# Kernel tuning notes

Hardware: AMD Instinct MI355X
Metric: run time of the kernel (lower is better)

The kernel has to match this reference:

```python
import jax, jax.numpy as jnp
import numpy as np

NUM_USERS = 60000
NUM_ITEMS = 40000
NUM_NODES = NUM_USERS + NUM_ITEMS
EMBED_DIM = 64
NUM_LAYERS = 3
NUM_EDGES = 1200000
BATCH = 16384


def setup_inputs() -> dict:
    key = jax.random.key(0)
    ks = jax.random.split(key, 7)
    user_indices = jax.random.randint(ks[0], (BATCH,), 0, NUM_USERS)
    item_indices = jax.random.randint(ks[1], (BATCH,), 0, NUM_ITEMS)
    edge_rows = jax.random.randint(ks[2], (NUM_EDGES,), 0, NUM_NODES)
    edge_cols = jax.random.randint(ks[3], (NUM_EDGES,), 0, NUM_NODES)
    # normalized adjacency values are small positives ~ 1/sqrt(deg_i*deg_j)
    edge_vals = jax.random.uniform(ks[4], (NUM_EDGES,), dtype=jnp.float32) * 0.1
    # xavier_uniform for Embedding(num, dim): bound = sqrt(6/(num+dim))
    bu = float(np.sqrt(6.0 / (NUM_USERS + EMBED_DIM)))
    bi = float(np.sqrt(6.0 / (NUM_ITEMS + EMBED_DIM)))
    user_emb = jax.random.uniform(ks[5], (NUM_USERS, EMBED_DIM), jnp.float32, -bu, bu)
    item_emb = jax.random.uniform(ks[6], (NUM_ITEMS, EMBED_DIM), jnp.float32, -bi, bi)
    return {
        "user_indices": user_indices,
        "item_indices": item_indices,
        "edge_rows": edge_rows,
        "edge_cols": edge_cols,
        "edge_vals": edge_vals,
        "user_emb": user_emb,
        "item_emb": item_emb,
    }


def _spmm(edge_rows, edge_cols, edge_vals, x):
    # out[i] = sum_{e: rows[e]==i} vals[e] * x[cols[e]]  -- COO SpMM
    msgs = edge_vals[:, None] * x[edge_cols]  # [E, D]
    return jax.ops.segment_sum(msgs, edge_rows, num_segments=NUM_NODES)


def reference(user_indices, item_indices, edge_rows, edge_cols, edge_vals,
              user_emb, item_emb):
    all_embeds = jnp.concatenate([user_emb, item_emb], axis=0)  # [N, D]
    for _ in range(NUM_LAYERS):
        all_embeds = _spmm(edge_rows, edge_cols, edge_vals, all_embeds)
    all_users = all_embeds[:NUM_USERS]
    all_items = all_embeds[NUM_USERS:]
    u = all_users[user_indices]  # [B, D]
    v = all_items[item_indices]  # [B, D]
    return jnp.sum(u * v, axis=1)  # [B]
```

## Files before the change

### kernel.cpp

```cpp
#include <hip/hip_runtime.h>

#define NUM_USERS 60000
#define NUM_ITEMS 40000
#define NUM_NODES 100000
#define DIM       64
#define NUM_EDGES 1200000
#define BATCH     16384

#define BROWS 128
#define NBUCK 782
#define CAP   2048
#define EPB   4096
#define NBINS 2048
#define NFLAGW 3125

__device__ __forceinline__ unsigned short f2bf(float f) {
    unsigned u = __float_as_uint(f);
    unsigned r = (u + 0x7FFFu + ((u >> 16) & 1u)) >> 16;
    return (unsigned short)r;
}

__global__ __launch_bounds__(256) void convert_emb(
    const float4* __restrict__ ue, const float4* __restrict__ ie,
    ushort4* __restrict__ xc)
{
    const int nU4 = NUM_USERS * (DIM / 4);
    const int total4 = NUM_NODES * (DIM / 4);
    int i = blockIdx.x * blockDim.x + threadIdx.x;
    int stride = gridDim.x * blockDim.x;
    for (; i < total4; i += stride) {
        float4 v = (i < nU4) ? ue[i] : ie[i - nU4];
        ushort4 s;
        s.x = f2bf(v.x); s.y = f2bf(v.y); s.z = f2bf(v.z); s.w = f2bf(v.w);
        xc[i] = s;
    }
}

__global__ __launch_bounds__(256) void bin_edges(
    const int* __restrict__ rows, const int* __restrict__ cols,
    const float* __restrict__ vals,
    const int* __restrict__ uidx, const int* __restrict__ iidx,
    int* __restrict__ gcursor, unsigned* __restrict__ flags,
    unsigned long long* __restrict__ tmp)
{
    __shared__ int cnt[NBUCK], lcur[NBUCK], gbase[NBUCK];
    int t = threadIdx.x;
    for (int i = t; i < NBUCK; i += 256) { cnt[i] = 0; lcur[i] = 0; }
    int fbase = blockIdx.x * 112;
    for (int k = t; k < 112; k += 256) {
        int gi = fbase + k;
        if (gi < BATCH) {
            int n = uidx[gi];
            atomicOr(&flags[n >> 5], 1u << (n & 31));
        } else if (gi < 2 * BATCH) {
            int n = NUM_USERS + iidx[gi - BATCH];
            atomicOr(&flags[n >> 5], 1u << (n & 31));
        }
    }
    __syncthreads();
    int base = blockIdx.x * EPB;
    int lim = NUM_EDGES - base; if (lim > EPB) lim = EPB;
    for (int k = t; k < lim; k += 256)
        atomicAdd(&cnt[rows[base + k] >> 7], 1);
    __syncthreads();
    for (int i = t; i < NBUCK; i += 256) {
        int c = cnt[i];
        gbase[i] = c ? atomicAdd(&gcursor[i], c) : 0;
    }
    __syncthreads();
    for (int k = t; k < lim; k += 256) {
        int idx = base + k;
        int r = rows[idx];
        int b = r >> 7;
        int lofs = atomicAdd(&lcur[b], 1);
        unsigned long long packed =
            ((unsigned long long)(unsigned)__float_as_int(vals[idx]) << 32)
            | ((unsigned)(r & 127) << 17) | (unsigned)cols[idx];
        tmp[(size_t)b * CAP + gbase[b] + lofs] = packed;
    }
}

__global__ __launch_bounds__(256) void sort_buckets(
    const unsigned long long* __restrict__ tmp, const int* __restrict__ gcursor,
    int2* __restrict__ rse, int2* __restrict__ csr)
{
    __shared__ int cnt[NBINS], cur[NBINS];
    __shared__ int sdata[256];
    __shared__ int2 stage[CAP];
    int b = blockIdx.x;
    int t = threadIdx.x;
    int count = gcursor[b];
    int base  = b * CAP;
    const unsigned long long* src = tmp + (size_t)base;
    for (int i = t; i < NBINS; i += 256) cnt[i] = 0;
    __syncthreads();
    for (int i = t; i < count; i += 256) {
        unsigned long long v = src[i];
        int lrow = (int)((v >> 17) & 127);
        int ct   = (int)((v & 0x1FFFF) >> 13);
        atomicAdd(&cnt[(lrow << 4) | ct], 1);
    }
    __syncthreads();
    int loc[8];
    int run = 0;
    #pragma unroll
    for (int j = 0; j < 8; ++j) { loc[j] = run; run += cnt[t * 8 + j]; }
    sdata[t] = run;
    __syncthreads();
    #pragma unroll
    for (int off = 1; off < 256; off <<= 1) {
        int x = (t >= off) ? sdata[t - off] : 0;
        __syncthreads();
        sdata[t] += x;
        __syncthreads();
    }
    int texcl = (t == 0) ? 0 : sdata[t - 1];
    #pragma unroll
    for (int j = 0; j < 8; ++j) cur[t * 8 + j] = texcl + loc[j];
    __syncthreads();
    if (t < BROWS) {
        int st = cur[t << 4];
        int en = (t < BROWS - 1) ? cur[(t + 1) << 4] : count;
        int row = b * BROWS + t;
        if (row < NUM_NODES)
            rse[row] = make_int2(base + st, base + en);
    }
    __syncthreads();
    for (int i = t; i < count; i += 256) {
        unsigned long long v = src[i];
        int lrow = (int)((v >> 17) & 127);
        int ct   = (int)((v & 0x1FFFF) >> 13);
        int pos = atomicAdd(&cur[(lrow << 4) | ct], 1);
        stage[pos] = make_int2((int)(v & 0x1FFFF), (int)(v >> 32));
    }
    __syncthreads();
    for (int i = t; i < count; i += 256)
        csr[(size_t)base + i] = stage[i];
}

__global__ __launch_bounds__(256) void compact_rows(
    const unsigned* __restrict__ flags, int* __restrict__ list,
    int* __restrict__ nrows)
{
    int i = blockIdx.x * blockDim.x + threadIdx.x;
    if (i < NUM_NODES && ((flags[i >> 5] >> (i & 31)) & 1u)) {
        int pos = atomicAdd(nrows, 1);
        list[pos] = i;
    }
}

__device__ __forceinline__ float4 bf16_row(const unsigned short* x16, int c, int q)
{
    ushort4 h = *(const ushort4*)(x16 + ((size_t)c << 6) + (q << 2));
    float4 f;
    f.x = __uint_as_float((unsigned)h.x << 16);
    f.y = __uint_as_float((unsigned)h.y << 16);
    f.z = __uint_as_float((unsigned)h.z << 16);
    f.w = __uint_as_float((unsigned)h.w << 16);
    return f;
}

__device__ __forceinline__ float4 row_accum_bf16(
    int e, int end, int q, const int2* __restrict__ csr,
    const unsigned short* __restrict__ x16)
{
    float4 acc = make_float4(0.f, 0.f, 0.f, 0.f);
    for (; e + 3 < end; e += 4) {
        int2 p0 = csr[e], p1 = csr[e + 1], p2 = csr[e + 2], p3 = csr[e + 3];
        float4 x0 = bf16_row(x16, p0.x, q);
        float4 x1 = bf16_row(x16, p1.x, q);
        float4 x2 = bf16_row(x16, p2.x, q);
        float4 x3 = bf16_row(x16, p3.x, q);
        float v0 = __int_as_float(p0.y), v1 = __int_as_float(p1.y);
        float v2 = __int_as_float(p2.y), v3 = __int_as_float(p3.y);
        acc.x = fmaf(v0, x0.x, acc.x); acc.y = fmaf(v0, x0.y, acc.y);
        acc.z = fmaf(v0, x0.z, acc.z); acc.w = fmaf(v0, x0.w, acc.w);
        acc.x = fmaf(v1, x1.x, acc.x); acc.y = fmaf(v1, x1.y, acc.y);
        acc.z = fmaf(v1, x1.z, acc.z); acc.w = fmaf(v1, x1.w, acc.w);
        acc.x = fmaf(v2, x2.x, acc.x); acc.y = fmaf(v2, x2.y, acc.y);
        acc.z = fmaf(v2, x2.z, acc.z); acc.w = fmaf(v2, x2.w, acc.w);
        acc.x = fmaf(v3, x3.x, acc.x); acc.y = fmaf(v3, x3.y, acc.y);
        acc.z = fmaf(v3, x3.z, acc.z); acc.w = fmaf(v3, x3.w, acc.w);
    }
    for (; e < end; ++e) {
        int2 p0 = csr[e];
        float4 x0 = bf16_row(x16, p0.x, q);
        float v = __int_as_float(p0.y);
        acc.x = fmaf(v, x0.x, acc.x); acc.y = fmaf(v, x0.y, acc.y);
        acc.z = fmaf(v, x0.z, acc.z); acc.w = fmaf(v, x0.w, acc.w);
    }
    return acc;
}

__global__ __launch_bounds__(256) void spmm_bb(
    const int2* __restrict__ rse, const int2* __restrict__ csr,
    const unsigned short* __restrict__ x16, unsigned short* __restrict__ y16)
{
    int tid = blockIdx.x * blockDim.x + threadIdx.x;
    int row = tid >> 4;
    if (row >= NUM_NODES) return;
    int q = tid & 15;
    int2 se = rse[row];
    float4 a = row_accum_bf16(se.x, se.y, q, csr, x16);
    ushort4 s;
    s.x = f2bf(a.x); s.y = f2bf(a.y); s.z = f2bf(a.z); s.w = f2bf(a.w);
    *(ushort4*)(y16 + ((size_t)row << 6) + (q << 2)) = s;
}

__global__ __launch_bounds__(256) void spmm_l3(
    const int* __restrict__ list, const int* __restrict__ nrows,
    const int2* __restrict__ rse, const int2* __restrict__ csr,
    const unsigned short* __restrict__ x16, float* __restrict__ y)
{
    int tid = blockIdx.x * blockDim.x + threadIdx.x;
    int i = tid >> 4;
    if (i >= *nrows) return;
    int q = tid & 15;
    int row = list[i];
    int2 se = rse[row];
    float4 acc = row_accum_bf16(se.x, se.y, q, csr, x16);
    ((float4*)y)[((size_t)row << 4) + q] = acc;
}

__global__ __launch_bounds__(256) void dot_kernel(
    const int*   __restrict__ uidx,
    const int*   __restrict__ iidx,
    const float* __restrict__ x,
    float*       __restrict__ out)
{
    int wid  = (blockIdx.x * blockDim.x + threadIdx.x) >> 6;
    int lane = threadIdx.x & 63;
    if (wid >= BATCH) return;
    int u  = uidx[wid];
    int it = iidx[wid];
    float a = x[(size_t)u * DIM + lane];
    float bb = x[((size_t)NUM_USERS + it) * DIM + lane];
    float p = a * bb;
    #pragma unroll
    for (int off = 32; off > 0; off >>= 1)
        p += __shfl_down(p, off);
    if (lane == 0) out[wid] = p;
}

extern "C" void kernel_launch(void* const* d_in, const int* in_sizes, int n_in,
                              void* d_out, int out_size, void* d_ws, size_t ws_size,
                              hipStream_t stream)
{
    const int*   user_indices = (const int*)  d_in[0];
    const int*   item_indices = (const int*)  d_in[1];
    const int*   edge_rows    = (const int*)  d_in[2];
    const int*   edge_cols    = (const int*)  d_in[3];
    const float* edge_vals    = (const float*)d_in[4];
    const float* user_emb     = (const float*)d_in[5];
    const float* item_emb     = (const float*)d_in[6];
    float*       out          = (float*)      d_out;

    const size_t nfloats = (size_t)NUM_NODES * DIM;
    char* p = (char*)d_ws;
    float* bufA = (float*)p;
    unsigned long long* tmp = (unsigned long long*)p;
    p += (size_t)NBUCK * CAP * 8;
    unsigned short* xc   = (unsigned short*)p;  p += nfloats * 2;
    unsigned short* b16B = (unsigned short*)p;  p += nfloats * 2;
    unsigned short* b16A = (unsigned short*)p;  p += nfloats * 2;
    int2*     rse     = (int2*)p;     p += 102400 * 8;
    int*      gcursor = (int*)p;      p += 1024 * 4;
    int*      nrows   = (int*)p;      p += 256 * 4;
    unsigned* flags   = (unsigned*)p; p += 3200 * 4;
    int*      rowlist = (int*)p;      p += 33024 * 4;
    int2*     csr     = (int2*)p;     p += (size_t)NBUCK * CAP * 8;

    const int NB_BIN = (NUM_EDGES + EPB - 1) / EPB;

    hipMemsetAsync(gcursor, 0, (1024 + 256 + 3200) * sizeof(int), stream);
    convert_emb<<<2048, 256, 0, stream>>>(
        (const float4*)user_emb, (const float4*)item_emb, (ushort4*)xc);
    bin_edges<<<NB_BIN, 256, 0, stream>>>(
        edge_rows, edge_cols, edge_vals, user_indices, item_indices,
        gcursor, flags, tmp);
    sort_buckets<<<NBUCK, 256, 0, stream>>>(tmp, gcursor, rse, csr);
    compact_rows<<<(NUM_NODES + 255) / 256, 256, 0, stream>>>(
        flags, rowlist, nrows);

    const int NB_SPMM = (NUM_NODES * 16 + 255) / 256;
    spmm_bb<<<NB_SPMM, 256, 0, stream>>>(rse, csr, xc, b16B);
    spmm_bb<<<NB_SPMM, 256, 0, stream>>>(rse, csr, b16B, b16A);
    spmm_l3<<<(32768 * 16) / 256, 256, 0, stream>>>(
        rowlist, nrows, rse, csr, b16A, bufA);

    dot_kernel<<<(BATCH * 64) / 256, 256, 0, stream>>>(
        user_indices, item_indices, bufA, out);
}
```

Measured before the change: 147.4 us.

## Use 256-row buckets, drop column sub-sort, fold memset into convert kernel

Doubles the rows per bucket to 256 (391 buckets, capacity 4096) and simplifies the bucket sort to a pure per-row counting sort, dropping the secondary column-tile ordering within each row. It replaces the separate hipMemsetAsync with zeroing done by block 0 of the conversion kernel, and runs the binning kernel with 512-thread blocks. This is meant to cut sorting work and launch overhead. In exchange, edges within a row are no longer ordered by column tile, which can hurt gather locality in the SpMM. The zeroing in convert_emb also relies on stream ordering before bin_edges, and the stage buffer grows to 32KB of LDS, which may limit occupancy of sort_buckets.

```diff
diff --git a/kernel.cpp b/kernel.cpp
--- a/kernel.cpp
+++ b/kernel.cpp
@@ -7,12 +7,12 @@
 #define NUM_EDGES 1200000
 #define BATCH     16384
 
-#define BROWS 128
-#define NBUCK 782
-#define CAP   2048
+#define BROWS 256
+#define NBUCK 391
+#define CAP   4096
 #define EPB   4096
-#define NBINS 2048
-#define NFLAGW 3125
+#define BINBLK 512
+#define ZWORDS (512 + 256 + 3200)
 
 __device__ __forceinline__ unsigned short f2bf(float f) {
     unsigned u = __float_as_uint(f);
@@ -22,8 +22,10 @@
 
 __global__ __launch_bounds__(256) void convert_emb(
     const float4* __restrict__ ue, const float4* __restrict__ ie,
-    ushort4* __restrict__ xc)
-{
+    ushort4* __restrict__ xc, int* __restrict__ zbase)
+{
+    if (blockIdx.x == 0)
+        for (int i = threadIdx.x; i < ZWORDS; i += 256) zbase[i] = 0;
     const int nU4 = NUM_USERS * (DIM / 4);
     const int total4 = NUM_NODES * (DIM / 4);
     int i = blockIdx.x * blockDim.x + threadIdx.x;
@@ -36,7 +38,7 @@
     }
 }
 
-__global__ __launch_bounds__(256) void bin_edges(
+__global__ __launch_bounds__(BINBLK) void bin_edges(
     const int* __restrict__ rows, const int* __restrict__ cols,
     const float* __restrict__ vals,
     const int* __restrict__ uidx, const int* __restrict__ iidx,
@@ -45,9 +47,9 @@
 {
     __shared__ int cnt[NBUCK], lcur[NBUCK], gbase[NBUCK];
     int t = threadIdx.x;
-    for (int i = t; i < NBUCK; i += 256) { cnt[i] = 0; lcur[i] = 0; }
+    for (int i = t; i < NBUCK; i += BINBLK) { cnt[i] = 0; lcur[i] = 0; }
     int fbase = blockIdx.x * 112;
-    for (int k = t; k < 112; k += 256) {
+    for (int k = t; k < 112; k += BINBLK) {
         int gi = fbase + k;
         if (gi < BATCH) {
             int n = uidx[gi];
@@ -60,22 +62,22 @@
     __syncthreads();
     int base = blockIdx.x * EPB;
     int lim = NUM_EDGES - base; if (lim > EPB) lim = EPB;
-    for (int k = t; k < lim; k += 256)
-        atomicAdd(&cnt[rows[base + k] >> 7], 1);
-    __syncthreads();
-    for (int i = t; i < NBUCK; i += 256) {
+    for (int k = t; k < lim; k += BINBLK)
+        atomicAdd(&cnt[rows[base + k] >> 8], 1);
+    __syncthreads();
+    for (int i = t; i < NBUCK; i += BINBLK) {
         int c = cnt[i];
         gbase[i] = c ? atomicAdd(&gcursor[i], c) : 0;
     }
     __syncthreads();
-    for (int k = t; k < lim; k += 256) {
+    for (int k = t; k < lim; k += BINBLK) {
         int idx = base + k;
         int r = rows[idx];
-        int b = r >> 7;
+        int b = r >> 8;
         int lofs = atomicAdd(&lcur[b], 1);
         unsigned long long packed =
             ((unsigned long long)(unsigned)__float_as_int(vals[idx]) << 32)
-            | ((unsigned)(r & 127) << 17) | (unsigned)cols[idx];
+            | ((unsigned)(r & 255) << 17) | (unsigned)cols[idx];
         tmp[(size_t)b * CAP + gbase[b] + lofs] = packed;
     }
 }
@@ -84,28 +86,20 @@
     const unsigned long long* __restrict__ tmp, const int* __restrict__ gcursor,
     int2* __restrict__ rse, int2* __restrict__ csr)
 {
-    __shared__ int cnt[NBINS], cur[NBINS];
-    __shared__ int sdata[256];
+    __shared__ int lcnt[BROWS], rowcur[BROWS], sdata[BROWS];
     __shared__ int2 stage[CAP];
     int b = blockIdx.x;
     int t = threadIdx.x;
     int count = gcursor[b];
     int base  = b * CAP;
     const unsigned long long* src = tmp + (size_t)base;
-    for (int i = t; i < NBINS; i += 256) cnt[i] = 0;
-    __syncthreads();
-    for (int i = t; i < count; i += 256) {
-        unsigned long long v = src[i];
-        int lrow = (int)((v >> 17) & 127);
-        int ct   = (int)((v & 0x1FFFF) >> 13);
-        atomicAdd(&cnt[(lrow << 4) | ct], 1);
-    }
-    __syncthreads();
-    int loc[8];
-    int run = 0;
-    #pragma unroll
-    for (int j = 0; j < 8; ++j) { loc[j] = run; run += cnt[t * 8 + j]; }
-    sdata[t] = run;
+    lcnt[t] = 0;
+    __syncthreads();
+    for (int i = t; i < count; i += 256)
+        atomicAdd(&lcnt[(int)((src[i] >> 17) & 255)], 1);
+    __syncthreads();
+    int myc = lcnt[t];
+    sdata[t] = myc;
     __syncthreads();
     #pragma unroll
     for (int off = 1; off < 256; off <<= 1) {
@@ -114,23 +108,16 @@
         sdata[t] += x;
         __syncthreads();
     }
-    int texcl = (t == 0) ? 0 : sdata[t - 1];
-    #pragma unroll
-    for (int j = 0; j < 8; ++j) cur[t * 8 + j] = texcl + loc[j];
-    __syncthreads();
-    if (t < BROWS) {
-        int st = cur[t << 4];
-        int en = (t < BROWS - 1) ? cur[(t + 1) << 4] : count;
-        int row = b * BROWS + t;
-        if (row < NUM_NODES)
-            rse[row] = make_int2(base + st, base + en);
-    }
+    int excl = sdata[t] - myc;
+    rowcur[t] = excl;
+    int row = b * BROWS + t;
+    if (row < NUM_NODES)
+        rse[row] = make_int2(base + excl, base + excl + myc);
     __syncthreads();
     for (int i = t; i < count; i += 256) {
         unsigned long long v = src[i];
-        int lrow = (int)((v >> 17) & 127);
-        int ct   = (int)((v & 0x1FFFF) >> 13);
-        int pos = atomicAdd(&cur[(lrow << 4) | ct], 1);
+        int lr = (int)((v >> 17) & 255);
+        int pos = atomicAdd(&rowcur[lr], 1);
         stage[pos] = make_int2((int)(v & 0x1FFFF), (int)(v >> 32));
     }
     __syncthreads();
@@ -208,13 +195,13 @@
 }
 
 __global__ __launch_bounds__(256) void spmm_l3(
-    const int* __restrict__ list, const int* __restrict__ nrows,
+    const int* __restrict__ list, const int* __restrict__ nrowsp,
     const int2* __restrict__ rse, const int2* __restrict__ csr,
     const unsigned short* __restrict__ x16, float* __restrict__ y)
 {
     int tid = blockIdx.x * blockDim.x + threadIdx.x;
     int i = tid >> 4;
-    if (i >= *nrows) return;
+    if (i >= *nrowsp) return;
     int q = tid & 15;
     int row = list[i];
     int2 se = rse[row];
@@ -264,7 +251,7 @@
     unsigned short* b16B = (unsigned short*)p;  p += nfloats * 2;
     unsigned short* b16A = (unsigned short*)p;  p += nfloats * 2;
     int2*     rse     = (int2*)p;     p += 102400 * 8;
-    int*      gcursor = (int*)p;      p += 1024 * 4;
+    int*      gcursor = (int*)p;      p += 512 * 4;
     int*      nrows   = (int*)p;      p += 256 * 4;
     unsigned* flags   = (unsigned*)p; p += 3200 * 4;
     int*      rowlist = (int*)p;      p += 33024 * 4;
@@ -272,10 +259,9 @@
 
     const int NB_BIN = (NUM_EDGES + EPB - 1) / EPB;
 
-    hipMemsetAsync(gcursor, 0, (1024 + 256 + 3200) * sizeof(int), stream);
     convert_emb<<<2048, 256, 0, stream>>>(
-        (const float4*)user_emb, (const float4*)item_emb, (ushort4*)xc);
-    bin_edges<<<NB_BIN, 256, 0, stream>>>(
+        (const float4*)user_emb, (const float4*)item_emb, (ushort4*)xc, gcursor);
+    bin_edges<<<NB_BIN, BINBLK, 0, stream>>>(
         edge_rows, edge_cols, edge_vals, user_indices, item_indices,
         gcursor, flags, tmp);
     sort_buckets<<<NBUCK, 256, 0, stream>>>(tmp, gcursor, rse, csr);
```

Measured after the change: 138.3 us. 6.2% less time.
